# Kernel tuning notes

Hardware: AMD Instinct MI355X
Metric: run time of the kernel (lower is better)

Reference implementation:

```python
import jax, jax.numpy as jnp
import numpy as np

NUM_FEATURES = 162  # 81 my-piece cells + 81 opponent cells
ACC = 1024          # accumulator_size
H1 = 32
H2 = 32
NB = 8              # num_buckets
DIV = 20            # bucket_divisor
BATCH = 32768


def _linear_init(key, fan_in, shape):
    bound = 1.0 / np.sqrt(fan_in)
    return jax.random.uniform(key, shape, minval=-bound, maxval=bound, dtype=jnp.float32)


def setup_inputs() -> dict:
    key = jax.random.key(0)
    ks = jax.random.split(key, 12)
    # sparse 0/1 board features with per-sample density so all buckets occur
    p = jax.random.uniform(ks[0], (BATCH, 1), minval=0.05, maxval=0.95)
    stm_features = (jax.random.uniform(ks[1], (BATCH, NUM_FEATURES)) < p).astype(jnp.float32)
    nstm_features = (jax.random.uniform(ks[2], (BATCH, NUM_FEATURES)) < p).astype(jnp.float32)
    W_acc = _linear_init(ks[3], NUM_FEATURES, (ACC + 1, NUM_FEATURES))
    b_acc = _linear_init(ks[4], NUM_FEATURES, (ACC + 1,))
    W1 = _linear_init(ks[5], 2 * ACC, (H1 * NB, 2 * ACC))
    b1 = _linear_init(ks[6], 2 * ACC, (H1 * NB,))
    W2 = _linear_init(ks[7], H1, (H2 * NB, H1))
    b2 = _linear_init(ks[8], H1, (H2 * NB,))
    W3 = _linear_init(ks[9], H2, (1 * NB, H2))
    b3 = _linear_init(ks[10], H2, (1 * NB,))
    return {
        "stm_features": stm_features, "nstm_features": nstm_features,
        "W_acc": W_acc, "b_acc": b_acc,
        "W1": W1, "b1": b1, "W2": W2, "b2": b2, "W3": W3, "b3": b3,
    }


def reference(stm_features, nstm_features, W_acc, b_acc, W1, b1, W2, b2, W3, b3):
    B = stm_features.shape[0]
    # accumulator (shared for both perspectives); last unit is PSQT
    raw_stm = stm_features @ W_acc.T + b_acc    # [B, ACC+1]
    raw_nstm = nstm_features @ W_acc.T + b_acc  # [B, ACC+1]
    hidden_stm, psqt_stm = raw_stm[:, :-1], raw_stm[:, -1]
    hidden_nstm, psqt_nstm = raw_nstm[:, :-1], raw_nstm[:, -1]
    # SCReLU: clipped [0,1] then squared
    act_stm = jnp.clip(hidden_stm, 0.0, 1.0) ** 2
    act_nstm = jnp.clip(hidden_nstm, 0.0, 1.0) ** 2
    x = jnp.concatenate([act_stm, act_nstm], axis=1)  # [B, 2*ACC]
    # bucket index from piece count of stm features
    piece_count = (stm_features[:, :81].sum(axis=1)
                   + stm_features[:, 81:162].sum(axis=1)).astype(jnp.int32)
    buckets = jnp.clip(piece_count // DIV, 0, NB - 1)  # [B]
    bsel = buckets[:, None, None]
    # layer stack: compute all buckets, gather selected one per sample
    h1_all = (x @ W1.T + b1).reshape(B, NB, H1)
    h1 = jnp.clip(jnp.take_along_axis(h1_all, bsel, axis=1)[:, 0], 0.0, 1.0)  # [B, H1]
    h2_all = (h1 @ W2.T + b2).reshape(B, NB, H2)
    h2 = jnp.clip(jnp.take_along_axis(h2_all, bsel, axis=1)[:, 0], 0.0, 1.0)  # [B, H2]
    out_all = (h2 @ W3.T + b3).reshape(B, NB, 1)
    ls_out = jnp.take_along_axis(out_all, bsel, axis=1)[:, 0, 0]  # [B]
    psqt = (psqt_stm - psqt_nstm) * 0.5
    return (ls_out + psqt)[:, None]  # [B, 1]
```

## Files before the change

### kernel.cpp

```cpp
#include <hip/hip_runtime.h>

typedef _Float16 f16;
typedef f16 f16x8 __attribute__((ext_vector_type(8)));
typedef float f32x4 __attribute__((ext_vector_type(4)));
typedef float f32x16 __attribute__((ext_vector_type(16)));

#define BATCH   32768
#define NF      162
#define ACCH    1024
#define KSL     192
#define NKS2    12
#define NB      8
#define DIVQ    20
#define TM      32
#define NT      256
#define NCH     128
#define NCHUNK  (ACCH/NCH)
#define MAXTILE (BATCH/TM + NB)

#define BINBLK  256
#define RPB     (BATCH / BINBLK)

#define WS_WACC16   0
#define WS_W116     (WS_WACC16 + ACCH*KSL*2)
#define WS_BUCKET   (WS_W116 + 256*2048*2)
#define WS_ORDER    (WS_BUCKET + BATCH*4)
#define WS_CNT      (WS_ORDER + BATCH*4)
#define WS_BASE     (WS_CNT + 64)
#define WS_PART     (WS_BASE + 64)
#define WS_BLKMAP   (WS_PART + BINBLK*NB*4)

#define LDS_BYTES   16512

__global__ __launch_bounds__(512) void k_prepbin(const float* __restrict__ stm,
                                                 const float* __restrict__ Wacc,
                                                 const float* __restrict__ W1,
                                                 int* __restrict__ bucket,
                                                 int* __restrict__ part,
                                                 f16* __restrict__ waccF,
                                                 f16* __restrict__ w1F)
{
    if (blockIdx.x < BINBLK) {
        __shared__ int hist[NB];
        int tid = threadIdx.x;
        if (tid < NB) hist[tid] = 0;
        __syncthreads();
        int wv = tid >> 6, ln = tid & 63;
        int rowbase = blockIdx.x * RPB + wv * (RPB / 8);
        for (int i = 0; i < RPB / 8; i++) {
            int row = rowbase + i;
            const float* rp = stm + (long)row * NF;
            float s = 0.f;
            for (int k = ln; k < NF; k += 64) s += rp[k];
            for (int off = 32; off > 0; off >>= 1) s += __shfl_down(s, off);
            if (ln == 0) {
                int pc = (int)(s + 0.5f);
                int b = pc / DIVQ; if (b > NB - 1) b = NB - 1;
                bucket[row] = b;
                atomicAdd(&hist[b], 1);
            }
        }
        __syncthreads();
        if (tid < NB) part[blockIdx.x * NB + tid] = hist[tid];
    } else {
        int tid = (blockIdx.x - BINBLK) * blockDim.x + threadIdx.x;
        int stride = (gridDim.x - BINBLK) * blockDim.x;
        for (int t = tid; t < ACCH * KSL; t += stride) {
            int e = t & 7, f = t >> 3;
            int n = f & 127, g = f >> 7;
            int kh = g & 1, h = g >> 1;
            int ks = h % NKS2, c = h / NKS2;
            int k = ks * 16 + kh * 8 + e;
            waccF[t] = (f16)((k < NF) ? Wacc[(c * 128 + n) * NF + k] : 0.f);
        }
        for (int f = tid; f < 256 * 2048 / 8; f += stride) {
            int n = f & 31, g = f >> 5;
            int l4b = g & 3, ks = (g >> 2) & 3, c = (g >> 4) & 7;
            int s = (g >> 7) & 1, bkt = g >> 8;
            int k0 = s * 1024 + c * 128 + ks * 32 + l4b * 8;
            const float* src = W1 + (long)(bkt * 32 + n) * 2048 + k0;
            float4 va = *(const float4*)(src);
            float4 vb = *(const float4*)(src + 4);
            f16x8 h;
            h[0]=(f16)va.x; h[1]=(f16)va.y; h[2]=(f16)va.z; h[3]=(f16)va.w;
            h[4]=(f16)vb.x; h[5]=(f16)vb.y; h[6]=(f16)vb.z; h[7]=(f16)vb.w;
            *(f16x8*)(w1F + (long)f * 8) = h;
        }
    }
}

__global__ __launch_bounds__(256) void k_scatter(const int* __restrict__ bucket,
                                                 const int* __restrict__ part,
                                                 int* __restrict__ order,
                                                 int* __restrict__ cnt,
                                                 int* __restrict__ base,
                                                 int* __restrict__ blkmap)
{
    __shared__ int tot[NB], bas[NB], pre[NB], lcur[NB];
    __shared__ int tstart[NB + 1];
    int tid = threadIdx.x, bid = blockIdx.x;
    int w = tid >> 6, ln = tid & 63;

    if (bid < BINBLK) {
        for (int b = w; b < NB; b += 4) {
            int j0 = ln * 4;
            int p0 = part[(j0 + 0) * NB + b];
            int p1 = part[(j0 + 1) * NB + b];
            int p2 = part[(j0 + 2) * NB + b];
            int p3 = part[(j0 + 3) * NB + b];
            int s4 = p0 + p1 + p2 + p3;
            int inc = s4;
            for (int off = 1; off < 64; off <<= 1) {
                int n = __shfl_up(inc, off);
                if (ln >= off) inc += n;
            }
            if (ln == 63) tot[b] = inc;
            int excg = inc - s4;
            int g = bid >> 2;
            int prr = __shfl(excg, g);
            int q0 = __shfl(p0, g), q1 = __shfl(p1, g), q2 = __shfl(p2, g);
            int r = bid & 3;
            if (r > 0) prr += q0;
            if (r > 1) prr += q1;
            if (r > 2) prr += q2;
            if (ln == 0) pre[b] = prr;
        }
        __syncthreads();
        if (tid == 0) {
            int a = 0;
            for (int q = 0; q < NB; q++) { bas[q] = a; a += tot[q]; }
            for (int q = 0; q < NB; q++) lcur[q] = bas[q] + pre[q];
        }
        __syncthreads();
        int blkstart = bid * RPB;
        for (int i = tid; i < RPB; i += 256) {
            int row = blkstart + i;
            int b = bucket[row];
            int pos = atomicAdd(&lcur[b], 1);
            order[pos] = row;
        }
    } else {
        for (int b = w; b < NB; b += 4) {
            int j0 = ln * 4;
            int s4 = part[(j0 + 0) * NB + b] + part[(j0 + 1) * NB + b]
                   + part[(j0 + 2) * NB + b] + part[(j0 + 3) * NB + b];
            for (int off = 32; off > 0; off >>= 1) s4 += __shfl_down(s4, off);
            if (ln == 0) tot[b] = s4;
        }
        __syncthreads();
        if (tid == 0) {
            int a = 0, t = 0;
            for (int q = 0; q < NB; q++) {
                base[q] = a; cnt[q] = tot[q]; a += tot[q];
                tstart[q] = t; t += (tot[q] + TM - 1) / TM;
            }
            tstart[NB] = t;
        }
        __syncthreads();
        for (int i = tid; i < MAXTILE; i += 256) {
            int v = -1;
            for (int q = 0; q < NB; q++)
                if (i >= tstart[q] && i < tstart[q + 1]) v = q | ((i - tstart[q]) << 4);
            blkmap[i] = v;
        }
    }
}

__global__ __launch_bounds__(NT, 2) void k_main(
    const float* __restrict__ stm, const float* __restrict__ nstm,
    const float* __restrict__ Wacc, const float* __restrict__ bacc,
    const float* __restrict__ b1, const float* __restrict__ W2,
    const float* __restrict__ b2, const float* __restrict__ W3,
    const float* __restrict__ b3,
    const f16* __restrict__ waccF, const f16* __restrict__ w1F,
    const int* __restrict__ cnt, const int* __restrict__ base,
    const int* __restrict__ order, const int* __restrict__ blkmap,
    float* __restrict__ out)
{
    int bm = blkmap[blockIdx.x];
    if (bm < 0) return;
    int bkt = bm & 15, tile = bm >> 4;
    int rowbase = base[bkt] + tile * TM;
    int nrows = cnt[bkt] - tile * TM; if (nrows > TM) nrows = TM;

    extern __shared__ __align__(16) char lds_raw[];
    f16* Xb  = (f16*)lds_raw;
    f16* h1s = (f16*)lds_raw;
    f16* h2s = (f16*)(lds_raw + TM * 40 * 2);
    float* psq = (float*)(lds_raw + 2 * TM * NCH * 2);

    int tid = threadIdx.x;
    int wv = tid >> 6, ln = tid & 63;
    int l15 = ln & 15, l4 = ln >> 4, l31 = ln & 31, kh = ln >> 5;
    int mt = wv >> 1, nh = wv & 1;
    int colc = wv * 32 + l31;

    int rowclamp = (l31 < nrows) ? l31 : (nrows - 1);
    int rowidx = order[rowbase + rowclamp];

    float bb1 = b1[bkt * 32 + nh * 16 + l15];
    f32x4 h1acc; h1acc[0] = h1acc[1] = h1acc[2] = h1acc[3] = bb1;

    const float* psqw = Wacc + (long)ACCH * NF;
    const f16x8* wfr  = (const f16x8*)waccF;
    const f16x8* w1fr = (const f16x8*)w1F;

    for (int s = 0; s < 2; s++) {
        const float* rp = (s ? nstm : stm) + (long)rowidx * NF;
        f16x8 af[NKS2];
        float pp = 0.f;
        #pragma unroll
        for (int ks = 0; ks < NKS2; ks++) {
            int k0 = ks * 16 + kh * 8;
            float v0=0.f,v1=0.f,v2=0.f,v3=0.f,v4=0.f,v5=0.f,v6=0.f,v7=0.f;
            if (k0 <= 152) {
                float2 a0 = *(const float2*)(rp + k0);
                float2 a1 = *(const float2*)(rp + k0 + 2);
                float2 a2 = *(const float2*)(rp + k0 + 4);
                float2 a3 = *(const float2*)(rp + k0 + 6);
                v0=a0.x; v1=a0.y; v2=a1.x; v3=a1.y;
                v4=a2.x; v5=a2.y; v6=a3.x; v7=a3.y;
                if (wv == 0) {
                    float4 pa = *(const float4*)(psqw + k0);
                    float4 pb = *(const float4*)(psqw + k0 + 4);
                    pp += v0*pa.x + v1*pa.y + v2*pa.z + v3*pa.w
                        + v4*pb.x + v5*pb.y + v6*pb.z + v7*pb.w;
                }
            } else if (k0 == 160) {
                float2 a0 = *(const float2*)(rp + 160);
                v0 = a0.x; v1 = a0.y;
                if (wv == 0) pp += v0*psqw[160] + v1*psqw[161];
            }
            f16x8 h;
            h[0]=(f16)v0; h[1]=(f16)v1; h[2]=(f16)v2; h[3]=(f16)v3;
            h[4]=(f16)v4; h[5]=(f16)v5; h[6]=(f16)v6; h[7]=(f16)v7;
            af[ks] = h;
        }
        if (wv == 0) {
            pp += __shfl_xor(pp, 32);
            if (kh == 0) {
                if (s) psq[l31] -= 0.5f * pp;
                else   psq[l31]  = 0.5f * pp;
            }
        }

        for (int c = 0; c < NCHUNK; c++) {
            float bias = bacc[c * NCH + colc];
            f32x16 acc;
            #pragma unroll
            for (int q = 0; q < 16; q++) acc[q] = bias;
            const f16x8* wp = wfr + ((c * NKS2) * 2 + kh) * 128 + colc;
            #pragma unroll
            for (int ks = 0; ks < NKS2; ks++) {
                f16x8 bf = wp[ks * 256];
                acc = __builtin_amdgcn_mfma_f32_32x32x16_f16(af[ks], bf, acc, 0, 0, 0);
            }
            f16* xb = Xb + (((s << 3) | c) & 1) * TM * NCH;
            #pragma unroll
            for (int reg = 0; reg < 16; reg++) {
                int rr = 4 * kh + (reg & 3) + 8 * (reg >> 2);
                float v = acc[reg];
                v = fminf(fmaxf(v, 0.f), 1.f);
                v = v * v;
                xb[rr * NCH + ((((colc >> 3) ^ (rr & 7)) << 3) | (colc & 7))] = (f16)v;
            }
            __syncthreads();
            const f16x8* w1p = w1fr + ((bkt * 2 + s) * 8 + c) * 512;
            #pragma unroll
            for (int ks = 0; ks < NCH / 32; ks++) {
                int s0 = ks * 4 + l4;
                int row = mt * 16 + l15;
                f16x8 a = *(const f16x8*)(xb + row * NCH + ((s0 ^ (row & 7)) << 3));
                f16x8 b = w1p[s0 * 32 + nh * 16 + l15];
                h1acc = __builtin_amdgcn_mfma_f32_16x16x32_f16(a, b, h1acc, 0, 0, 0);
            }
        }
    }
    __syncthreads();

    #pragma unroll
    for (int jr = 0; jr < 4; jr++) {
        int row = mt * 16 + l4 * 4 + jr;
        int col = nh * 16 + l15;
        float v = fminf(fmaxf(h1acc[jr], 0.f), 1.f);
        h1s[row * 40 + col] = (f16)v;
    }
    __syncthreads();

    {
        int nn = nh * 16 + l15;
        const float* w2r = W2 + (bkt * 32 + nn) * 32;
        float4 wa = *(const float4*)(w2r + l4 * 8);
        float4 wb = *(const float4*)(w2r + l4 * 8 + 4);
        f16x8 bfr;
        bfr[0]=(f16)wa.x; bfr[1]=(f16)wa.y; bfr[2]=(f16)wa.z; bfr[3]=(f16)wa.w;
        bfr[4]=(f16)wb.x; bfr[5]=(f16)wb.y; bfr[6]=(f16)wb.z; bfr[7]=(f16)wb.w;
        int row = mt * 16 + l15;
        f16x8 a = *(const f16x8*)(h1s + row * 40 + l4 * 8);
        float bb2 = b2[bkt * 32 + nn];
        f32x4 acc2; acc2[0] = acc2[1] = acc2[2] = acc2[3] = bb2;
        acc2 = __builtin_amdgcn_mfma_f32_16x16x32_f16(a, bfr, acc2, 0, 0, 0);
        #pragma unroll
        for (int jr = 0; jr < 4; jr++) {
            int r2 = mt * 16 + l4 * 4 + jr;
            float v = fminf(fmaxf(acc2[jr], 0.f), 1.f);
            h2s[r2 * 40 + nn] = (f16)v;
        }
    }
    __syncthreads();

    if (tid < nrows) {
        const float* w3r = W3 + bkt * 32;
        float o = b3[bkt] + psq[tid];
        #pragma unroll 8
        for (int n = 0; n < 32; n++) o += (float)h2s[tid * 40 + n] * w3r[n];
        out[order[rowbase + tid]] = o;
    }
}

extern "C" void kernel_launch(void* const* d_in, const int* in_sizes, int n_in,
                              void* d_out, int out_size, void* d_ws, size_t ws_size,
                              hipStream_t stream)
{
    (void)in_sizes; (void)n_in; (void)out_size; (void)ws_size;
    const float* stm  = (const float*)d_in[0];
    const float* nstm = (const float*)d_in[1];
    const float* Wacc = (const float*)d_in[2];
    const float* bacc = (const float*)d_in[3];
    const float* W1   = (const float*)d_in[4];
    const float* b1   = (const float*)d_in[5];
    const float* W2   = (const float*)d_in[6];
    const float* b2   = (const float*)d_in[7];
    const float* W3   = (const float*)d_in[8];
    const float* b3   = (const float*)d_in[9];
    float* out = (float*)d_out;

    char* ws = (char*)d_ws;
    f16* waccF  = (f16*)(ws + WS_WACC16);
    f16* w1F    = (f16*)(ws + WS_W116);
    int* bucket = (int*)(ws + WS_BUCKET);
    int* order  = (int*)(ws + WS_ORDER);
    int* cnt    = (int*)(ws + WS_CNT);
    int* basep  = (int*)(ws + WS_BASE);
    int* part   = (int*)(ws + WS_PART);
    int* blkmap = (int*)(ws + WS_BLKMAP);

    hipLaunchKernelGGL(k_prepbin, dim3(1024), dim3(512), 0, stream,
                       stm, Wacc, W1, bucket, part, waccF, w1F);
    hipLaunchKernelGGL(k_scatter, dim3(BINBLK + 1), dim3(256), 0, stream,
                       bucket, part, order, cnt, basep, blkmap);

    hipFuncSetAttribute(reinterpret_cast<const void*>(k_main),
                        hipFuncAttributeMaxDynamicSharedMemorySize, LDS_BYTES);
    hipLaunchKernelGGL(k_main, dim3(MAXTILE), dim3(NT), LDS_BYTES, stream,
                       stm, nstm, Wacc, bacc, b1, W2, b2, W3, b3,
                       waccF, w1F, cnt, basep, order, blkmap, out);
}
```

Baseline: 186.1 us.

## Fuse binning into prep kernel and widen accumulator chunks to 256 columns

```diff
diff --git a/kernel.cpp b/kernel.cpp
--- a/kernel.cpp
+++ b/kernel.cpp
@@ -14,58 +14,65 @@
 #define DIVQ    20
 #define TM      32
 #define NT      256
-#define NCH     128
-#define NCHUNK  (ACCH/NCH)
+#define NCH2    256
 #define MAXTILE (BATCH/TM + NB)
-
-#define BINBLK  256
-#define RPB     (BATCH / BINBLK)
+#define REG     8192
+
+#define PBINBLK 64
+#define PRPB    (BATCH / PBINBLK)
+#define PGRID   512
 
 #define WS_WACC16   0
 #define WS_W116     (WS_WACC16 + ACCH*KSL*2)
-#define WS_BUCKET   (WS_W116 + 256*2048*2)
-#define WS_ORDER    (WS_BUCKET + BATCH*4)
-#define WS_CNT      (WS_ORDER + BATCH*4)
-#define WS_BASE     (WS_CNT + 64)
-#define WS_PART     (WS_BASE + 64)
-#define WS_BLKMAP   (WS_PART + BINBLK*NB*4)
-
-#define LDS_BYTES   16512
-
-__global__ __launch_bounds__(512) void k_prepbin(const float* __restrict__ stm,
-                                                 const float* __restrict__ Wacc,
-                                                 const float* __restrict__ W1,
-                                                 int* __restrict__ bucket,
-                                                 int* __restrict__ part,
-                                                 f16* __restrict__ waccF,
-                                                 f16* __restrict__ w1F)
+#define WS_ORDER    (WS_W116 + 256*2048*2)
+#define WS_CNT      (WS_ORDER + NB*REG*4)
+
+#define LDS_BYTES   32768
+
+__global__ __launch_bounds__(512) void k_prep(const float* __restrict__ stm,
+                                              const float* __restrict__ Wacc,
+                                              const float* __restrict__ W1,
+                                              int* __restrict__ cnt,
+                                              int* __restrict__ order,
+                                              f16* __restrict__ waccF,
+                                              f16* __restrict__ w1F)
 {
-    if (blockIdx.x < BINBLK) {
-        __shared__ int hist[NB];
-        int tid = threadIdx.x;
+    int tid = threadIdx.x, bid = blockIdx.x;
+    if (bid < PBINBLK) {
+        __shared__ int bkt_l[PRPB];
+        __shared__ int hist[NB], gb[NB];
         if (tid < NB) hist[tid] = 0;
         __syncthreads();
         int wv = tid >> 6, ln = tid & 63;
-        int rowbase = blockIdx.x * RPB + wv * (RPB / 8);
-        for (int i = 0; i < RPB / 8; i++) {
-            int row = rowbase + i;
-            const float* rp = stm + (long)row * NF;
-            float s = 0.f;
-            for (int k = ln; k < NF; k += 64) s += rp[k];
-            for (int off = 32; off > 0; off >>= 1) s += __shfl_down(s, off);
+        int rb = wv * (PRPB / 8);
+        int rowbase = bid * PRPB;
+        for (int i = 0; i < PRPB / 8; i++) {
+            int lrow = rb + i;
+            const float* rp = stm + (long)(rowbase + lrow) * NF;
+            float s2 = 0.f;
+            for (int k = ln; k < NF; k += 64) s2 += rp[k];
+            for (int off = 32; off > 0; off >>= 1) s2 += __shfl_down(s2, off);
             if (ln == 0) {
-                int pc = (int)(s + 0.5f);
+                int pc = (int)(s2 + 0.5f);
                 int b = pc / DIVQ; if (b > NB - 1) b = NB - 1;
-                bucket[row] = b;
+                bkt_l[lrow] = b;
                 atomicAdd(&hist[b], 1);
             }
         }
         __syncthreads();
-        if (tid < NB) part[blockIdx.x * NB + tid] = hist[tid];
+        if (tid < NB) gb[tid] = atomicAdd(&cnt[tid], hist[tid]);
+        __syncthreads();
+        if (tid < NB) hist[tid] = gb[tid];
+        __syncthreads();
+        for (int i = tid; i < PRPB; i += 512) {
+            int b = bkt_l[i];
+            int pos = atomicAdd(&hist[b], 1);
+            if (pos < REG) order[b * REG + pos] = rowbase + i;
+        }
     } else {
-        int tid = (blockIdx.x - BINBLK) * blockDim.x + threadIdx.x;
-        int stride = (gridDim.x - BINBLK) * blockDim.x;
-        for (int t = tid; t < ACCH * KSL; t += stride) {
+        int t0 = (bid - PBINBLK) * 512 + tid;
+        const int STRIDE = (PGRID - PBINBLK) * 512;
+        for (int t = t0; t < ACCH * KSL; t += STRIDE) {
             int e = t & 7, f = t >> 3;
             int n = f & 127, g = f >> 7;
             int kh = g & 1, h = g >> 1;
@@ -73,7 +80,7 @@
             int k = ks * 16 + kh * 8 + e;
             waccF[t] = (f16)((k < NF) ? Wacc[(c * 128 + n) * NF + k] : 0.f);
         }
-        for (int f = tid; f < 256 * 2048 / 8; f += stride) {
+        for (int f = t0; f < 256 * 2048 / 8; f += STRIDE) {
             int n = f & 31, g = f >> 5;
             int l4b = g & 3, ks = (g >> 2) & 3, c = (g >> 4) & 7;
             int s = (g >> 7) & 1, bkt = g >> 8;
@@ -89,83 +96,6 @@
     }
 }
 
-__global__ __launch_bounds__(256) void k_scatter(const int* __restrict__ bucket,
-                                                 const int* __restrict__ part,
-                                                 int* __restrict__ order,
-                                                 int* __restrict__ cnt,
-                                                 int* __restrict__ base,
-                                                 int* __restrict__ blkmap)
-{
-    __shared__ int tot[NB], bas[NB], pre[NB], lcur[NB];
-    __shared__ int tstart[NB + 1];
-    int tid = threadIdx.x, bid = blockIdx.x;
-    int w = tid >> 6, ln = tid & 63;
-
-    if (bid < BINBLK) {
-        for (int b = w; b < NB; b += 4) {
-            int j0 = ln * 4;
-            int p0 = part[(j0 + 0) * NB + b];
-            int p1 = part[(j0 + 1) * NB + b];
-            int p2 = part[(j0 + 2) * NB + b];
-            int p3 = part[(j0 + 3) * NB + b];
-            int s4 = p0 + p1 + p2 + p3;
-            int inc = s4;
-            for (int off = 1; off < 64; off <<= 1) {
-                int n = __shfl_up(inc, off);
-                if (ln >= off) inc += n;
-            }
-            if (ln == 63) tot[b] = inc;
-            int excg = inc - s4;
-            int g = bid >> 2;
-            int prr = __shfl(excg, g);
-            int q0 = __shfl(p0, g), q1 = __shfl(p1, g), q2 = __shfl(p2, g);
-            int r = bid & 3;
-            if (r > 0) prr += q0;
-            if (r > 1) prr += q1;
-            if (r > 2) prr += q2;
-            if (ln == 0) pre[b] = prr;
-        }
-        __syncthreads();
-        if (tid == 0) {
-            int a = 0;
-            for (int q = 0; q < NB; q++) { bas[q] = a; a += tot[q]; }
-            for (int q = 0; q < NB; q++) lcur[q] = bas[q] + pre[q];
-        }
-        __syncthreads();
-        int blkstart = bid * RPB;
-        for (int i = tid; i < RPB; i += 256) {
-            int row = blkstart + i;
-            int b = bucket[row];
-            int pos = atomicAdd(&lcur[b], 1);
-            order[pos] = row;
-        }
-    } else {
-        for (int b = w; b < NB; b += 4) {
-            int j0 = ln * 4;
-            int s4 = part[(j0 + 0) * NB + b] + part[(j0 + 1) * NB + b]
-                   + part[(j0 + 2) * NB + b] + part[(j0 + 3) * NB + b];
-            for (int off = 32; off > 0; off >>= 1) s4 += __shfl_down(s4, off);
-            if (ln == 0) tot[b] = s4;
-        }
-        __syncthreads();
-        if (tid == 0) {
-            int a = 0, t = 0;
-            for (int q = 0; q < NB; q++) {
-                base[q] = a; cnt[q] = tot[q]; a += tot[q];
-                tstart[q] = t; t += (tot[q] + TM - 1) / TM;
-            }
-            tstart[NB] = t;
-        }
-        __syncthreads();
-        for (int i = tid; i < MAXTILE; i += 256) {
-            int v = -1;
-            for (int q = 0; q < NB; q++)
-                if (i >= tstart[q] && i < tstart[q + 1]) v = q | ((i - tstart[q]) << 4);
-            blkmap[i] = v;
-        }
-    }
-}
-
 __global__ __launch_bounds__(NT, 2) void k_main(
     const float* __restrict__ stm, const float* __restrict__ nstm,
     const float* __restrict__ Wacc, const float* __restrict__ bacc,
@@ -173,21 +103,26 @@
     const float* __restrict__ b2, const float* __restrict__ W3,
     const float* __restrict__ b3,
     const f16* __restrict__ waccF, const f16* __restrict__ w1F,
-    const int* __restrict__ cnt, const int* __restrict__ base,
-    const int* __restrict__ order, const int* __restrict__ blkmap,
+    const int* __restrict__ cnt, const int* __restrict__ order,
     float* __restrict__ out)
 {
-    int bm = blkmap[blockIdx.x];
-    if (bm < 0) return;
-    int bkt = bm & 15, tile = bm >> 4;
-    int rowbase = base[bkt] + tile * TM;
-    int nrows = cnt[bkt] - tile * TM; if (nrows > TM) nrows = TM;
+    int t = blockIdx.x;
+    int bkt = -1, tile = 0, cb = 0, acc0i = 0;
+    #pragma unroll
+    for (int b = 0; b < NB; b++) {
+        int cbv = cnt[b];
+        int nb = (cbv + TM - 1) / TM;
+        if (bkt < 0 && t < acc0i + nb) { bkt = b; tile = t - acc0i; cb = cbv; }
+        acc0i += nb;
+    }
+    if (bkt < 0) return;
+    int rowbase = bkt * REG + tile * TM;
+    int nrows = cb - tile * TM; if (nrows > TM) nrows = TM;
 
     extern __shared__ __align__(16) char lds_raw[];
     f16* Xb  = (f16*)lds_raw;
     f16* h1s = (f16*)lds_raw;
     f16* h2s = (f16*)(lds_raw + TM * 40 * 2);
-    float* psq = (float*)(lds_raw + 2 * TM * NCH * 2);
 
     int tid = threadIdx.x;
     int wv = tid >> 6, ln = tid & 63;
@@ -199,11 +134,13 @@
     int rowidx = order[rowbase + rowclamp];
 
     float bb1 = b1[bkt * 32 + nh * 16 + l15];
-    f32x4 h1acc; h1acc[0] = h1acc[1] = h1acc[2] = h1acc[3] = bb1;
+    f32x4 h1a; h1a[0] = h1a[1] = h1a[2] = h1a[3] = bb1;
+    f32x4 h1b; h1b[0] = h1b[1] = h1b[2] = h1b[3] = 0.f;
 
     const float* psqw = Wacc + (long)ACCH * NF;
     const f16x8* wfr  = (const f16x8*)waccF;
     const f16x8* w1fr = (const f16x8*)w1F;
+    float psqr = 0.f;
 
     for (int s = 0; s < 2; s++) {
         const float* rp = (s ? nstm : stm) + (long)rowidx * NF;
@@ -238,41 +175,45 @@
         }
         if (wv == 0) {
             pp += __shfl_xor(pp, 32);
-            if (kh == 0) {
-                if (s) psq[l31] -= 0.5f * pp;
-                else   psq[l31]  = 0.5f * pp;
-            }
-        }
-
-        for (int c = 0; c < NCHUNK; c++) {
-            float bias = bacc[c * NCH + colc];
-            f32x16 acc;
-            #pragma unroll
-            for (int q = 0; q < 16; q++) acc[q] = bias;
-            const f16x8* wp = wfr + ((c * NKS2) * 2 + kh) * 128 + colc;
+            psqr += s ? (-0.5f * pp) : (0.5f * pp);
+        }
+
+        for (int C = 0; C < 4; C++) {
+            int oc0 = 2 * C, oc1 = 2 * C + 1;
+            float bias0 = bacc[oc0 * 128 + colc];
+            float bias1 = bacc[oc1 * 128 + colc];
+            f32x16 a0, a1;
+            #pragma unroll
+            for (int q = 0; q < 16; q++) { a0[q] = bias0; a1[q] = bias1; }
+            const f16x8* wp0 = wfr + ((oc0 * NKS2) * 2 + kh) * 128 + colc;
+            const f16x8* wp1 = wfr + ((oc1 * NKS2) * 2 + kh) * 128 + colc;
             #pragma unroll
             for (int ks = 0; ks < NKS2; ks++) {
-                f16x8 bf = wp[ks * 256];
-                acc = __builtin_amdgcn_mfma_f32_32x32x16_f16(af[ks], bf, acc, 0, 0, 0);
-            }
-            f16* xb = Xb + (((s << 3) | c) & 1) * TM * NCH;
+                f16x8 bf0 = wp0[ks * 256];
+                a0 = __builtin_amdgcn_mfma_f32_32x32x16_f16(af[ks], bf0, a0, 0, 0, 0);
+                f16x8 bf1 = wp1[ks * 256];
+                a1 = __builtin_amdgcn_mfma_f32_32x32x16_f16(af[ks], bf1, a1, 0, 0, 0);
+            }
+            f16* xb = Xb + (((s << 2) | C) & 1) * TM * NCH2;
             #pragma unroll
             for (int reg = 0; reg < 16; reg++) {
                 int rr = 4 * kh + (reg & 3) + 8 * (reg >> 2);
-                float v = acc[reg];
-                v = fminf(fmaxf(v, 0.f), 1.f);
-                v = v * v;
-                xb[rr * NCH + ((((colc >> 3) ^ (rr & 7)) << 3) | (colc & 7))] = (f16)v;
+                int xc0 = colc, xc1 = 128 + colc;
+                float v = fminf(fmaxf(a0[reg], 0.f), 1.f);
+                xb[rr * NCH2 + ((((xc0 >> 3) ^ rr) & 31) << 3) + (xc0 & 7)] = (f16)(v * v);
+                float w = fminf(fmaxf(a1[reg], 0.f), 1.f);
+                xb[rr * NCH2 + ((((xc1 >> 3) ^ rr) & 31) << 3) + (xc1 & 7)] = (f16)(w * w);
             }
             __syncthreads();
-            const f16x8* w1p = w1fr + ((bkt * 2 + s) * 8 + c) * 512;
-            #pragma unroll
-            for (int ks = 0; ks < NCH / 32; ks++) {
+            const f16x8* w1p = w1fr + (((bkt * 2 + s) * 8) + 2 * C) * 512;
+            int row = mt * 16 + l15;
+            #pragma unroll
+            for (int ks = 0; ks < 8; ks++) {
                 int s0 = ks * 4 + l4;
-                int row = mt * 16 + l15;
-                f16x8 a = *(const f16x8*)(xb + row * NCH + ((s0 ^ (row & 7)) << 3));
-                f16x8 b = w1p[s0 * 32 + nh * 16 + l15];
-                h1acc = __builtin_amdgcn_mfma_f32_16x16x32_f16(a, b, h1acc, 0, 0, 0);
+                f16x8 a = *(const f16x8*)(xb + row * NCH2 + (((s0 ^ row) & 31) << 3));
+                f16x8 b = w1p[ks * 128 + l4 * 32 + nh * 16 + l15];
+                if (ks & 1) h1b = __builtin_amdgcn_mfma_f32_16x16x32_f16(a, b, h1b, 0, 0, 0);
+                else        h1a = __builtin_amdgcn_mfma_f32_16x16x32_f16(a, b, h1a, 0, 0, 0);
             }
         }
     }
@@ -282,7 +223,7 @@
     for (int jr = 0; jr < 4; jr++) {
         int row = mt * 16 + l4 * 4 + jr;
         int col = nh * 16 + l15;
-        float v = fminf(fmaxf(h1acc[jr], 0.f), 1.f);
+        float v = fminf(fmaxf(h1a[jr] + h1b[jr], 0.f), 1.f);
         h1s[row * 40 + col] = (f16)v;
     }
     __syncthreads();
@@ -311,10 +252,10 @@
 
     if (tid < nrows) {
         const float* w3r = W3 + bkt * 32;
-        float o = b3[bkt] + psq[tid];
+        float o = b3[bkt] + psqr;
         #pragma unroll 8
         for (int n = 0; n < 32; n++) o += (float)h2s[tid * 40 + n] * w3r[n];
-        out[order[rowbase + tid]] = o;
+        out[rowidx] = o;
     }
 }
 
@@ -338,21 +279,16 @@
     char* ws = (char*)d_ws;
     f16* waccF  = (f16*)(ws + WS_WACC16);
     f16* w1F    = (f16*)(ws + WS_W116);
-    int* bucket = (int*)(ws + WS_BUCKET);
     int* order  = (int*)(ws + WS_ORDER);
     int* cnt    = (int*)(ws + WS_CNT);
-    int* basep  = (int*)(ws + WS_BASE);
-    int* part   = (int*)(ws + WS_PART);
-    int* blkmap = (int*)(ws + WS_BLKMAP);
-
-    hipLaunchKernelGGL(k_prepbin, dim3(1024), dim3(512), 0, stream,
-                       stm, Wacc, W1, bucket, part, waccF, w1F);
-    hipLaunchKernelGGL(k_scatter, dim3(BINBLK + 1), dim3(256), 0, stream,
-                       bucket, part, order, cnt, basep, blkmap);
+
+    hipMemsetAsync(cnt, 0, NB * sizeof(int), stream);
+    hipLaunchKernelGGL(k_prep, dim3(PGRID), dim3(512), 0, stream,
+                       stm, Wacc, W1, cnt, order, waccF, w1F);
 
     hipFuncSetAttribute(reinterpret_cast<const void*>(k_main),
                         hipFuncAttributeMaxDynamicSharedMemorySize, LDS_BYTES);
     hipLaunchKernelGGL(k_main, dim3(MAXTILE), dim3(NT), LDS_BYTES, stream,
                        stm, nstm, Wacc, bacc, b1, W2, b2, W3, b3,
-                       waccF, w1F, cnt, basep, order, blkmap, out);
+                       waccF, w1F, cnt, order, out);
 }
```

Result: slower. 277.1 us (+48.9%).
